# Optimization experiments

Measured on AMD Instinct MI355X. Metric: run time of the kernel, lower is better.

Reference implementation:

```python
import jax, jax.numpy as jnp
import numpy as np

N_HEAD = 16
DIM_K = 64
DIM_MODEL = N_HEAD * DIM_K  # 1024; seq_len is forced to equal dim_model by the reshape
SCALE = float(DIM_K ** 0.5)


def setup_inputs() -> dict:
    key = jax.random.key(0)
    ks = jax.random.split(key, 4)
    B, S, D = 32, DIM_MODEL, 1024
    x = jax.random.normal(ks[0], (B, S, D), dtype=jnp.float32)
    glorot = float(1.0 / np.sqrt(D))
    Wq = jax.random.normal(ks[1], (D, DIM_MODEL), dtype=jnp.float32) * glorot
    Wk = jax.random.normal(ks[2], (D, DIM_MODEL), dtype=jnp.float32) * glorot
    Wv = jax.random.normal(ks[3], (D, DIM_MODEL), dtype=jnp.float32) * glorot
    bq = jnp.zeros((DIM_MODEL,), jnp.float32)
    bk = jnp.zeros((DIM_MODEL,), jnp.float32)
    bv = jnp.zeros((DIM_MODEL,), jnp.float32)
    return {"x": x, "Wq": Wq, "bq": bq, "Wk": Wk, "bk": bk, "Wv": Wv, "bv": bv}


def reference(x, Wq, bq, Wk, bk, Wv, bv):
    # x: [B, S, D] with S == DIM_MODEL (required by the original reshape)
    B = x.shape[0]
    q = x @ Wq + bq  # [B, S, dm]
    k = x @ Wk + bk
    v = x @ Wv + bv
    # TF1 K.batch_dot(q, k, axes=[-1,-1]) -> tf.matmul(q, k, adjoint_a=True):
    # contracts over the SEQUENCE axis -> [B, dm, dm]
    y = jnp.einsum('bsd,bse->bde', q, k) / SCALE
    # softmax over dim_k-sized chunks of the last axis
    y = y.reshape(B, DIM_MODEL, N_HEAD, DIM_K)
    y = jax.nn.softmax(y, axis=-1)
    y = y.reshape(B, DIM_MODEL, DIM_MODEL)
    # TF1 K.batch_dot(v, y, axes=[2,3]) -> tf.matmul(v, y) (no adjoints)
    out = jnp.einsum('bsd,bde->bse', v, y)  # [B, S, dm]
    return out
```

## Files before the change

kernel.cpp:

```cpp
#include <hip/hip_runtime.h>
#include <hip/hip_bf16.h>

#define DM 1024
#define NB 32

typedef __bf16 bf16_t;
typedef __attribute__((ext_vector_type(8))) __bf16 bf16x8;
typedef __attribute__((ext_vector_type(4))) float  f32x4;

__device__ inline float bf2f(bf16_t v) {
    union { unsigned short s; __bf16 b; } u; u.b = v;
    union { unsigned int i; float f; } w; w.i = ((unsigned int)u.s) << 16;
    return w.f;
}
__device__ inline bf16_t f2bf(float f) {
    union { unsigned int i; float f; } w; w.f = f;
    unsigned int r = (w.i + 0x7FFFu + ((w.i >> 16) & 1u)) >> 16;
    union { unsigned short s; __bf16 b; } u; u.s = (unsigned short)r;
    return u.b;
}

enum EpiMode { EPI_NONE = 0, EPI_BIAS_ROW = 1, EPI_BIAS_COL = 2, EPI_SCALE = 3 };

__global__ void detect_mode(const unsigned short* __restrict__ x, int* __restrict__ mode)
{
    if (threadIdx.x == 0 && blockIdx.x == 0) {
        int hits = 0;
        for (int i = 0; i < 2048; ++i) {
            unsigned e = (x[i] >> 7) & 0xFFu;
            hits += (e >= 0x8Du) ? 1 : 0;
        }
        *mode = (hits >= 16) ? 1 : 0;
    }
}

__global__ void convert_x(const void* __restrict__ xin, bf16_t* __restrict__ xb,
                          const int* __restrict__ modep, long long off, long long n8)
{
    const long long i = (long long)blockIdx.x * blockDim.x + threadIdx.x;
    if (i >= n8) return;
    bf16x8 o;
    if (*modep) {
        const float* s = (const float*)xin + off + i * 8;
#pragma unroll
        for (int j = 0; j < 8; ++j) o[j] = f2bf(s[j]);
    } else {
        o = *(const bf16x8*)((const bf16_t*)xin + off + i * 8);
    }
    *(bf16x8*)(xb + i * 8) = o;
}

__global__ void transpose3(const void* __restrict__ Wq, const void* __restrict__ Wk,
                           const void* __restrict__ Wv, bf16_t* __restrict__ Wt,
                           const int* __restrict__ modep)
{
    const int md = *modep;
    const void* src = (blockIdx.z == 0) ? Wq : (blockIdx.z == 1) ? Wk : Wv;
    bf16_t* dst = Wt + (size_t)blockIdx.z * DM * DM;
    __shared__ bf16_t T[64][72];
    const int tid = threadIdx.x;
    const int r  = tid >> 2;
    const int cp = tid & 3;
    const int r0 = blockIdx.y * 64;
    const int c0 = blockIdx.x * 64;
    const size_t base = (size_t)(r0 + r) * DM + c0 + cp * 16;
    bf16_t tmp[16];
    if (md) {
        const float* s = (const float*)src + base;
#pragma unroll
        for (int j = 0; j < 16; ++j) tmp[j] = f2bf(s[j]);
    } else {
        const bf16_t* s = (const bf16_t*)src + base;
        bf16x8 a = *(const bf16x8*)s;
        bf16x8 b = *(const bf16x8*)(s + 8);
#pragma unroll
        for (int j = 0; j < 8; ++j) { tmp[j] = a[j]; tmp[8 + j] = b[j]; }
    }
#pragma unroll
    for (int j = 0; j < 16; ++j) T[cp * 16 + j][r] = tmp[j];
    __syncthreads();
    bf16_t* d = dst + (size_t)(c0 + r) * DM + r0 + cp * 16;
    bf16x8 w0, w1;
#pragma unroll
    for (int j = 0; j < 8; ++j) w0[j] = T[r][cp * 16 + j];
#pragma unroll
    for (int j = 0; j < 8; ++j) w1[j] = T[r][cp * 16 + 8 + j];
    *(bf16x8*)d = w0;
    *(bf16x8*)(d + 8) = w1;
}

template <int MODE, bool DUALOUT>
__global__ __launch_bounds__(256, 2)
void gemm_nt(const bf16_t* __restrict__ A, long long sA,
             const bf16_t* __restrict__ B, long long sB,
             void* __restrict__ C, long long sC, long long cOff,
             const void* __restrict__ bias, const int* __restrict__ modep,
             int M, int N, int K, float scale)
{
    constexpr int BM = 128, BN = 128, BK = 64;
    __shared__ __align__(16) bf16_t As[BM * BK];
    __shared__ __align__(16) bf16_t Bs[BN * BK];

    const int z = blockIdx.z;
    const bf16_t* Ab = A + (size_t)z * (size_t)sA;
    const bf16_t* Bb = B + (size_t)z * (size_t)sB;

    const int gm0 = blockIdx.y * BM;
    const int gn0 = blockIdx.x * BN;

    const int tid  = threadIdx.x;
    const int wave = tid >> 6;
    const int lane = tid & 63;
    const int wm   = (wave >> 1) * 64;
    const int wn   = (wave & 1) * 64;
    const int lm   = lane & 15;
    const int quad = lane >> 4;

    f32x4 acc[4][4];
#pragma unroll
    for (int i = 0; i < 4; ++i)
#pragma unroll
        for (int j = 0; j < 4; ++j) acc[i][j] = (f32x4)0.0f;

    const int nIter = K / BK;
    bf16x8 rA[4], rB[4];

    auto gload = [&](int it) {
#pragma unroll
        for (int i = 0; i < 4; ++i) {
            const int ch = tid + i * 256;
            const int row = ch >> 3, kc = ch & 7;
            rA[i] = *(const bf16x8*)(Ab + (size_t)(gm0 + row) * K + it * BK + kc * 8);
            rB[i] = *(const bf16x8*)(Bb + (size_t)(gn0 + row) * K + it * BK + kc * 8);
        }
    };
    auto swrite = [&]() {
#pragma unroll
        for (int i = 0; i < 4; ++i) {
            const int ch = tid + i * 256;
            const int row = ch >> 3, kc = ch & 7;
            *(bf16x8*)&As[row * BK + kc * 8] = rA[i];
            *(bf16x8*)&Bs[row * BK + kc * 8] = rB[i];
        }
    };

    gload(0);

    for (int it = 0; it < nIter; ++it) {
        __syncthreads();
        swrite();
        __syncthreads();
        if (it + 1 < nIter) gload(it + 1);
#pragma unroll
        for (int kh = 0; kh < 2; ++kh) {
            bf16x8 af[4], bg[4];
#pragma unroll
            for (int mt = 0; mt < 4; ++mt) {
                const int m = wm + mt * 16 + lm;
                af[mt] = *(const bf16x8*)&As[m * BK + (kh * 4 + quad) * 8];
            }
#pragma unroll
            for (int nt = 0; nt < 4; ++nt) {
                const int n = wn + nt * 16 + lm;
                bg[nt] = *(const bf16x8*)&Bs[n * BK + (kh * 4 + quad) * 8];
            }
#pragma unroll
            for (int mt = 0; mt < 4; ++mt)
#pragma unroll
                for (int nt = 0; nt < 4; ++nt)
                    acc[mt][nt] = __builtin_amdgcn_mfma_f32_16x16x32_bf16(
                        af[mt], bg[nt], acc[mt][nt], 0, 0, 0);
        }
    }

    const int md = *modep;
#pragma unroll
    for (int mt = 0; mt < 4; ++mt) {
        float rbias[4];
        if (MODE == EPI_BIAS_ROW) {
#pragma unroll
            for (int r = 0; r < 4; ++r) {
                const int i = gm0 + wm + mt * 16 + quad * 4 + r;
                rbias[r] = md ? ((const float*)bias)[i] : bf2f(((const bf16_t*)bias)[i]);
            }
        }
#pragma unroll
        for (int nt = 0; nt < 4; ++nt) {
            const int col = gn0 + wn + nt * 16 + lm;
            float cbias = 0.f;
            if (MODE == EPI_BIAS_COL)
                cbias = md ? ((const float*)bias)[col] : bf2f(((const bf16_t*)bias)[col]);
#pragma unroll
            for (int r = 0; r < 4; ++r) {
                const int row = gm0 + wm + mt * 16 + quad * 4 + r;
                float v = acc[mt][nt][r];
                if (MODE == EPI_BIAS_ROW) v += rbias[r];
                if (MODE == EPI_BIAS_COL) v += cbias;
                if (MODE == EPI_SCALE)    v *= scale;
                const size_t off = (size_t)cOff + (size_t)z * sC + (size_t)row * N + col;
                if (DUALOUT && md) ((float*)C)[off] = v;
                else               ((bf16_t*)C)[off] = f2bf(v);
            }
        }
    }
}

__global__ void softmax_t_inplace(bf16_t* __restrict__ Y)
{
    const int b = blockIdx.z;
    int idx = blockIdx.x;
    int I = 0;
    while (idx >= 16 - I) { idx -= 16 - I; ++I; }
    const int J = I + idx;

    const int tid = threadIdx.x;
    const int r  = tid >> 2;
    const int cp = tid & 3;

    bf16_t* base = Y + ((size_t)b << 20);
    bf16_t* t0 = base + (size_t)(I * 64 + r) * DM + J * 64 + cp * 16;
    bf16_t* t1 = base + (size_t)(J * 64 + r) * DM + I * 64 + cp * 16;

    __shared__ bf16_t P0[64][72];
    __shared__ bf16_t P1[64][72];

    bf16x8 a0 = *(const bf16x8*)t0;
    bf16x8 a1 = *(const bf16x8*)(t0 + 8);
    bf16x8 c0v, c1v;
    if (J != I) { c0v = *(const bf16x8*)t1; c1v = *(const bf16x8*)(t1 + 8); }

    {
        float f[16];
#pragma unroll
        for (int j = 0; j < 8; ++j) f[j] = bf2f(a0[j]);
#pragma unroll
        for (int j = 0; j < 8; ++j) f[8 + j] = bf2f(a1[j]);
        float m = -1e30f;
#pragma unroll
        for (int j = 0; j < 16; ++j) m = fmaxf(m, f[j]);
        m = fmaxf(m, __shfl_xor(m, 1));
        m = fmaxf(m, __shfl_xor(m, 2));
        float s = 0.f;
#pragma unroll
        for (int j = 0; j < 16; ++j) { f[j] = __expf(f[j] - m); s += f[j]; }
        s += __shfl_xor(s, 1);
        s += __shfl_xor(s, 2);
        const float inv = 1.0f / s;
#pragma unroll
        for (int j = 0; j < 16; ++j) P0[cp * 16 + j][r] = f2bf(f[j] * inv);
    }
    if (J != I) {
        float f[16];
#pragma unroll
        for (int j = 0; j < 8; ++j) f[j] = bf2f(c0v[j]);
#pragma unroll
        for (int j = 0; j < 8; ++j) f[8 + j] = bf2f(c1v[j]);
        float m = -1e30f;
#pragma unroll
        for (int j = 0; j < 16; ++j) m = fmaxf(m, f[j]);
        m = fmaxf(m, __shfl_xor(m, 1));
        m = fmaxf(m, __shfl_xor(m, 2));
        float s = 0.f;
#pragma unroll
        for (int j = 0; j < 16; ++j) { f[j] = __expf(f[j] - m); s += f[j]; }
        s += __shfl_xor(s, 1);
        s += __shfl_xor(s, 2);
        const float inv = 1.0f / s;
#pragma unroll
        for (int j = 0; j < 16; ++j) P1[cp * 16 + j][r] = f2bf(f[j] * inv);
    }
    __syncthreads();

    bf16x8 w0, w1;
#pragma unroll
    for (int j = 0; j < 8; ++j) w0[j] = P0[r][cp * 16 + j];
#pragma unroll
    for (int j = 0; j < 8; ++j) w1[j] = P0[r][cp * 16 + 8 + j];
    *(bf16x8*)t1 = w0;
    *(bf16x8*)(t1 + 8) = w1;
    if (J != I) {
#pragma unroll
        for (int j = 0; j < 8; ++j) w0[j] = P1[r][cp * 16 + j];
#pragma unroll
        for (int j = 0; j < 8; ++j) w1[j] = P1[r][cp * 16 + 8 + j];
        *(bf16x8*)t0 = w0;
        *(bf16x8*)(t0 + 8) = w1;
    }
}

extern "C" void kernel_launch(void* const* d_in, const int* in_sizes, int n_in,
                              void* d_out, int out_size, void* d_ws, size_t ws_size,
                              hipStream_t stream)
{
    const void* x  = d_in[0];
    const void* Wq = d_in[1];
    const void* bq = d_in[2];
    const void* Wk = d_in[3];
    const void* bk = d_in[4];
    const void* Wv = d_in[5];
    const void* bv = d_in[6];

    char* ws = (char*)d_ws;
    int* mode = (int*)ws;
    const size_t MB2 = (size_t)DM * DM * 2;
    const size_t hdr = 256;
    int CB = NB;
    while (CB > 1 && hdr + 3 * MB2 + 4 * (size_t)CB * MB2 > ws_size) CB >>= 1;

    bf16_t* Wt = (bf16_t*)(ws + hdr);
    bf16_t* xb = (bf16_t*)(ws + hdr + 3 * MB2);
    bf16_t* qt = xb + (size_t)CB * DM * DM;
    bf16_t* kt = qt + (size_t)CB * DM * DM;
    bf16_t* y  = kt + (size_t)CB * DM * DM;
    bf16_t* v  = qt;

    detect_mode<<<1, 64, 0, stream>>>((const unsigned short*)x, mode);
    transpose3<<<dim3(16, 16, 3), 256, 0, stream>>>(Wq, Wk, Wv, Wt, mode);

    const long long msz = (long long)DM * DM;
    for (int c = 0; c < NB; c += CB) {
        const int zb = (NB - c < CB) ? (NB - c) : CB;
        const long long n8 = (long long)zb * msz / 8;
        convert_x<<<(int)((n8 + 255) / 256), 256, 0, stream>>>(x, xb, mode, (long long)c * msz, n8);

        const dim3 g(8, 8, zb), blk(256);
        gemm_nt<EPI_BIAS_ROW, false><<<g, blk, 0, stream>>>(Wt, 0, xb, msz, qt, msz, 0, bq, mode, DM, DM, DM, 1.f);
        gemm_nt<EPI_BIAS_ROW, false><<<g, blk, 0, stream>>>(Wt + msz, 0, xb, msz, kt, msz, 0, bk, mode, DM, DM, DM, 1.f);
        gemm_nt<EPI_SCALE, false><<<g, blk, 0, stream>>>(qt, msz, kt, msz, y, msz, 0, nullptr, mode, DM, DM, DM, 0.125f);
        softmax_t_inplace<<<dim3(136, 1, zb), 256, 0, stream>>>(y);
        gemm_nt<EPI_BIAS_COL, false><<<g, blk, 0, stream>>>(xb, msz, Wt + 2 * msz, 0, v, msz, 0, bv, mode, DM, DM, DM, 1.f);
        gemm_nt<EPI_NONE, true><<<g, blk, 0, stream>>>(v, msz, y, msz, d_out, msz, (long long)c * msz, nullptr, mode, DM, DM, DM, 1.f);
    }
}
```

Baseline: 799.8 us.

## Load GEMM tiles directly into LDS and remap workgroups across XCDs

Replaces the register-staged global-to-LDS copy with direct global_load_lds transfers, which removes the VGPR round trip and the separate LDS write pass. It also remaps workgroup IDs so consecutive tiles are grouped per XCD, aiming for better L2 locality. The new loop issues the load and then consumes it in the same iteration with no prefetch of the next tile, so the previous overlap of global loads with MFMA is lost. Correctness depends on __syncthreads also waiting for the async LDS loads (vmcnt).

```diff
diff --git a/kernel.cpp b/kernel.cpp
--- a/kernel.cpp
+++ b/kernel.cpp
@@ -7,6 +7,13 @@
 typedef __bf16 bf16_t;
 typedef __attribute__((ext_vector_type(8))) __bf16 bf16x8;
 typedef __attribute__((ext_vector_type(4))) float  f32x4;
+
+typedef __attribute__((address_space(1))) void gas_void;
+typedef __attribute__((address_space(3))) void las_void;
+
+__device__ __forceinline__ void async_lds16(const bf16_t* g, bf16_t* l) {
+    __builtin_amdgcn_global_load_lds((gas_void*)g, (las_void*)l, 16, 0, 0);
+}
 
 __device__ inline float bf2f(bf16_t v) {
     union { unsigned short s; __bf16 b; } u; u.b = v;
@@ -101,12 +108,23 @@
     __shared__ __align__(16) bf16_t As[BM * BK];
     __shared__ __align__(16) bf16_t Bs[BN * BK];
 
-    const int z = blockIdx.z;
+    const int Gx = gridDim.x, Gy = gridDim.y;
+    const int nwg = Gx * Gy * (int)gridDim.z;
+    int bx = blockIdx.x, by = blockIdx.y, z = blockIdx.z;
+    if ((nwg & 7) == 0) {
+        const int orig = bx + Gx * (by + Gy * z);
+        const int nper = nwg >> 3;
+        const int nid  = (orig & 7) * nper + (orig >> 3);
+        bx = nid % Gx;
+        by = (nid / Gx) % Gy;
+        z  = nid / (Gx * Gy);
+    }
+
     const bf16_t* Ab = A + (size_t)z * (size_t)sA;
     const bf16_t* Bb = B + (size_t)z * (size_t)sB;
 
-    const int gm0 = blockIdx.y * BM;
-    const int gn0 = blockIdx.x * BN;
+    const int gm0 = by * BM;
+    const int gn0 = bx * BN;
 
     const int tid  = threadIdx.x;
     const int wave = tid >> 6;
@@ -123,34 +141,23 @@
         for (int j = 0; j < 4; ++j) acc[i][j] = (f32x4)0.0f;
 
     const int nIter = K / BK;
-    bf16x8 rA[4], rB[4];
-
-    auto gload = [&](int it) {
+
+    auto stage = [&](int it) {
 #pragma unroll
         for (int i = 0; i < 4; ++i) {
             const int ch = tid + i * 256;
             const int row = ch >> 3, kc = ch & 7;
-            rA[i] = *(const bf16x8*)(Ab + (size_t)(gm0 + row) * K + it * BK + kc * 8);
-            rB[i] = *(const bf16x8*)(Bb + (size_t)(gn0 + row) * K + it * BK + kc * 8);
+            async_lds16(Ab + (size_t)(gm0 + row) * K + it * BK + kc * 8,
+                        As + ch * 8);
+            async_lds16(Bb + (size_t)(gn0 + row) * K + it * BK + kc * 8,
+                        Bs + ch * 8);
         }
     };
-    auto swrite = [&]() {
-#pragma unroll
-        for (int i = 0; i < 4; ++i) {
-            const int ch = tid + i * 256;
-            const int row = ch >> 3, kc = ch & 7;
-            *(bf16x8*)&As[row * BK + kc * 8] = rA[i];
-            *(bf16x8*)&Bs[row * BK + kc * 8] = rB[i];
-        }
-    };
-
-    gload(0);
 
     for (int it = 0; it < nIter; ++it) {
+        if (it != 0) __syncthreads();
+        stage(it);
         __syncthreads();
-        swrite();
-        __syncthreads();
-        if (it + 1 < nIter) gload(it + 1);
 #pragma unroll
         for (int kh = 0; kh < 2; ++kh) {
             bf16x8 af[4], bg[4];
```

Result: faster. 762.8 us (-4.6%).
